# Optimization experiments

Measured on AMD Instinct MI355X. Metric: run time of the kernel, lower is better.

The kernel has to match this reference:

```python
import jax, jax.numpy as jnp
import numpy as np

K, T, D, H = 256, 256, 64, 256
TEMP = 1.0
LOG2 = float(np.log(2.0))


def setup_inputs() -> dict:
    key = jax.random.key(0)
    k1, k2, k3, k4 = jax.random.split(key, 4)
    embeddings_KxtxD = jax.random.normal(k1, (K, T, D), dtype=jnp.float32)
    leaf_counts_Kxt = jax.random.randint(k2, (K, T), 0, 3).astype(jnp.int32)
    W1 = jax.random.normal(k3, (2 * D, H), dtype=jnp.float32) * 0.05
    b1 = jnp.zeros((H,), dtype=jnp.float32)
    W2 = jax.random.normal(k4, (H, D), dtype=jnp.float32) * 0.05
    b2 = jnp.zeros((D,), dtype=jnp.float32)
    return {"N": 256, "leaf_counts_Kxt": leaf_counts_Kxt,
            "embeddings_KxtxD": embeddings_KxtxD, "log": 0,
            "W1": W1, "b1": b1, "W2": W2, "b2": b2}


def _pairwise_dist(emb):  # [K,t,D] -> [K,t,t] Euclidean, no KxtxtxD blowup
    sq = jnp.sum(emb * emb, axis=-1)                       # [K,t]
    gram = jnp.einsum('ktd,ksd->kts', emb, emb)            # [K,t,t]
    d2 = sq[:, :, None] + sq[:, None, :] - 2.0 * gram
    return jnp.sqrt(jnp.maximum(d2, 0.0))


def reference(N, leaf_counts_Kxt, embeddings_KxtxD, log, W1, b1, W2, b2):
    k, t = leaf_counts_Kxt.shape
    dist_Kxtxt = _pairwise_dist(embeddings_KxtxD)
    logw_Kxtxt = -dist_Kxtxt / TEMP
    eye = jnp.eye(t, dtype=bool)
    logw_Kxtxt = jnp.where(eye[None], -jnp.inf, logw_Kxtxt)  # diagonal_scatter(-inf)

    # categorical sample over flattened t*t logits (Gumbel-max)
    skey = jax.random.key(42)
    g = jax.random.gumbel(skey, (k, t * t), dtype=jnp.float32)
    flat_logw = logw_Kxtxt.reshape(k, t * t)
    flat_sample_K = jnp.argmax(flat_logw + g, axis=-1)
    idx1_K = flat_sample_K // t
    idx2_K = flat_sample_K % t

    rows = jnp.arange(k)
    child1_KxD = embeddings_KxtxD[rows, idx1_K]            # gather_K
    child2_KxD = embeddings_KxtxD[rows, idx2_K]

    # merge encoder MLP
    h = jax.nn.relu(jnp.concatenate([child1_KxD, child2_KxD], axis=-1) @ W1 + b1)
    embedding_KxD = h @ W2 + b2

    # sample_branches=False: branch length = distance(child, merged)
    branch1_K = jnp.linalg.norm(child1_KxD - embedding_KxD, axis=-1)
    branch2_K = jnp.linalg.norm(child2_KxD - embedding_KxD, axis=-1)

    log_merge_prob_K = logw_Kxtxt[rows, idx1_K, idx2_K]    # gather_K2
    log_merge_prob_K = log_merge_prob_K + LOG2
    log_merge_prob_K = log_merge_prob_K - jax.scipy.special.logsumexp(
        logw_Kxtxt, axis=(1, 2))
    log_v_plus_K = log_merge_prob_K  # branch priors are 0

    ones_K = jnp.sum((leaf_counts_Kxt == 1).astype(jnp.int32), axis=1)
    ones_K = ones_K - (leaf_counts_Kxt[rows, idx1_K] == 1).astype(jnp.int32)
    ones_K = ones_K - (leaf_counts_Kxt[rows, idx2_K] == 1).astype(jnp.int32)
    v_minus_K = N - ones_K
    log_v_minus_K = jnp.log(v_minus_K.astype(jnp.float32))

    return (idx1_K, idx2_K, branch1_K, branch2_K, embedding_KxD,
            log_v_plus_K, log_v_minus_K)
```

## Files before the change

### kernel.cpp

```cpp
#include <hip/hip_runtime.h>
#include <stdint.h>
#include <math.h>

#define TK 256
#define TT 256
#define DD 64
#define HH 256
#define NTHREADS 1024
#define PADB 72

typedef short bf16x8 __attribute__((ext_vector_type(8)));
typedef float f32x4  __attribute__((ext_vector_type(4)));

struct KWs { unsigned long long packed; float ss; unsigned int arrive; unsigned int pad; };

__device__ __forceinline__ uint32_t rotl32(uint32_t x, uint32_t d) {
  return (x << d) | (x >> (32u - d));
}
__device__ __forceinline__ uint2 threefry2x32(uint32_t x0, uint32_t x1) {
  const uint32_t ks0 = 0u, ks1 = 42u, ks2 = 0x1BD11BF0u;
  x0 += ks0; x1 += ks1;
#define TFR(r) { x0 += x1; x1 = rotl32(x1, r); x1 ^= x0; }
  TFR(13u) TFR(15u) TFR(26u) TFR(6u)
  x0 += ks1; x1 += ks2 + 1u;
  TFR(17u) TFR(29u) TFR(16u) TFR(24u)
  x0 += ks2; x1 += ks0 + 2u;
  TFR(13u) TFR(15u) TFR(26u) TFR(6u)
  x0 += ks0; x1 += ks1 + 3u;
  TFR(17u) TFR(29u) TFR(16u) TFR(24u)
  x0 += ks1; x1 += ks2 + 4u;
  TFR(13u) TFR(15u) TFR(26u) TFR(6u)
  x0 += ks2; x1 += ks0 + 5u;
#undef TFR
  return make_uint2(x0, x1);
}

__device__ __forceinline__ uint16_t f2bf(float x) {
  uint32_t u = __float_as_uint(x);
  return (uint16_t)((u + 0x7FFFu + ((u >> 16) & 1u)) >> 16);
}

__global__ __launch_bounds__(NTHREADS) void ep_fused(
    const int*   __restrict__ pN,
    const int*   __restrict__ leaf,
    const float* __restrict__ emb,
    const float* __restrict__ W1,
    const float* __restrict__ b1,
    const float* __restrict__ W2,
    const float* __restrict__ b2,
    float*       __restrict__ out,
    KWs*         __restrict__ ws)
{
  __shared__ uint16_t s_hi[TT * PADB];
  __shared__ uint16_t s_lo[TT * PADB];
  __shared__ float s_sq[TT];
  __shared__ float s_c1[DD], s_c2[DD];
  __shared__ float s_wss[16], s_wb[16];
  __shared__ int   s_wi[16], s_onesw[16], s_sel[2];
  __shared__ float s_h[HH], s_e[DD];
  __shared__ float s_lse;
  __shared__ int   s_exec;

  const int k    = blockIdx.x >> 1;
  const int half = blockIdx.x & 1;
  const int tid  = threadIdx.x;
  const float* ek = emb + (size_t)k * (TT * DD);

  for (int idx = tid; idx < TT * DD / 4; idx += NTHREADS) {
    float4 v = ((const float4*)ek)[idx];
    int f = idx << 2;
    int r = f >> 6, c = f & 63;
    uint16_t h0 = f2bf(v.x), h1 = f2bf(v.y), h2 = f2bf(v.z), h3 = f2bf(v.w);
    float l0f = v.x - __uint_as_float((uint32_t)h0 << 16);
    float l1f = v.y - __uint_as_float((uint32_t)h1 << 16);
    float l2f = v.z - __uint_as_float((uint32_t)h2 << 16);
    float l3f = v.w - __uint_as_float((uint32_t)h3 << 16);
    uint2 hp = make_uint2((uint32_t)h0 | ((uint32_t)h1 << 16),
                          (uint32_t)h2 | ((uint32_t)h3 << 16));
    uint2 lp = make_uint2((uint32_t)f2bf(l0f) | ((uint32_t)f2bf(l1f) << 16),
                          (uint32_t)f2bf(l2f) | ((uint32_t)f2bf(l3f) << 16));
    *(uint2*)&s_hi[r * PADB + c] = hp;
    *(uint2*)&s_lo[r * PADB + c] = lp;
  }
  if (tid < TT) {
    const float* row = ek + tid * DD;
    float acc = 0.f;
#pragma unroll
    for (int c = 0; c < DD; ++c) acc = fmaf(row[c], row[c], acc);
    s_sq[tid] = acc;
  }
  __syncthreads();

  const int wv = tid >> 6, l = tid & 63;
  const int lm = l & 15, lk = l >> 4;
  const int I0 = wv * 16;

  const char* hib = (const char*)s_hi;
  const char* lob = (const char*)s_lo;
  const int arow = (I0 + lm) * (PADB * 2);
  bf16x8 ah0 = *(const bf16x8*)(hib + arow + lk * 16);
  bf16x8 ah1 = *(const bf16x8*)(hib + arow + 64 + lk * 16);
  bf16x8 al0 = *(const bf16x8*)(lob + arow + lk * 16);
  bf16x8 al1 = *(const bf16x8*)(lob + arow + 64 + lk * 16);

  float sqi_r[4];
#pragma unroll
  for (int r = 0; r < 4; ++r) sqi_r[r] = s_sq[I0 + lk * 4 + r];

  float ss = 0.f, best = -3.402823466e38f;
  int bidx = 0x7fffffff;

  for (int jt = half * 8; jt < half * 8 + 8; ++jt) {
    const int J0 = jt * 16;
    const int brow = (J0 + lm) * (PADB * 2);
    bf16x8 bh0 = *(const bf16x8*)(hib + brow + lk * 16);
    bf16x8 bh1 = *(const bf16x8*)(hib + brow + 64 + lk * 16);
    bf16x8 bl0 = *(const bf16x8*)(lob + brow + lk * 16);
    bf16x8 bl1 = *(const bf16x8*)(lob + brow + 64 + lk * 16);

    f32x4 acc = {0.f, 0.f, 0.f, 0.f};
    acc = __builtin_amdgcn_mfma_f32_16x16x32_bf16(ah0, bh0, acc, 0, 0, 0);
    acc = __builtin_amdgcn_mfma_f32_16x16x32_bf16(ah0, bl0, acc, 0, 0, 0);
    acc = __builtin_amdgcn_mfma_f32_16x16x32_bf16(al0, bh0, acc, 0, 0, 0);
    acc = __builtin_amdgcn_mfma_f32_16x16x32_bf16(ah1, bh1, acc, 0, 0, 0);
    acc = __builtin_amdgcn_mfma_f32_16x16x32_bf16(ah1, bl1, acc, 0, 0, 0);
    acc = __builtin_amdgcn_mfma_f32_16x16x32_bf16(al1, bh1, acc, 0, 0, 0);

    const int j = J0 + lm;
    const float sqj = s_sq[j];
    const uint32_t pbase = ((uint32_t)k << 16) | (uint32_t)j;

#pragma unroll
    for (int r = 0; r < 4; ++r) {
      const int i = I0 + lk * 4 + r;
      float dsq = sqi_r[r] + sqj - 2.0f * acc[r];
      float lw  = -sqrtf(fmaxf(dsq, 0.f));
      if (i != j) {
        ss += __expf(lw);
        uint2 rr = threefry2x32(0u, pbase + ((uint32_t)i << 8));
        uint32_t bits = rr.x ^ rr.y;
        float f = __uint_as_float((bits >> 9) | 0x3F800000u) - 1.0f;
        float u = fmaxf(f, 1.1754943508222875e-38f);
        float g = -__logf(-__logf(u));
        float sv = lw + g;
        int fi = i * TT + j;
        if (sv > best || (sv == best && fi < bidx)) { best = sv; bidx = fi; }
      }
    }
  }

#pragma unroll
  for (int off = 32; off > 0; off >>= 1) {
    ss += __shfl_xor(ss, off);
    float ob = __shfl_xor(best, off);
    int   oi = __shfl_xor(bidx, off);
    if (ob > best || (ob == best && oi < bidx)) { best = ob; bidx = oi; }
  }
  if (l == 0) { s_wss[wv] = ss; s_wb[wv] = best; s_wi[wv] = bidx; }
  {
    int isone = (tid < TT) ? ((leaf[k * TT + tid] == 1) ? 1 : 0) : 0;
    unsigned long long bal = __ballot(isone);
    if (l == 0) s_onesw[wv] = __popcll(bal);
  }
  __syncthreads();

  if (tid == 0) {
    float tot = 0.f, bb = -3.402823466e38f; int bi = 0x7fffffff;
    for (int w = 0; w < 16; ++w) {
      tot += s_wss[w];
      if (s_wb[w] > bb || (s_wb[w] == bb && s_wi[w] < bi)) { bb = s_wb[w]; bi = s_wi[w]; }
    }
    KWs* w = ws + k;
    uint32_t sb = __float_as_uint(bb);
    uint32_t mapped = (sb & 0x80000000u) ? ~sb : (sb | 0x80000000u);
    unsigned long long pk = ((unsigned long long)mapped << 32) |
                            (unsigned long long)(~(uint32_t)bi);
    atomicAdd(&w->ss, tot);
    atomicMax(&w->packed, pk);
    __threadfence();
    unsigned int old = atomicAdd(&w->arrive, 1u);
    if (old == 1u) {
      float tt = atomicAdd(&w->ss, 0.0f);
      unsigned long long fp = atomicMax(&w->packed, 0ull);
      int fbi = (int)(~(uint32_t)(fp & 0xFFFFFFFFull));
      s_sel[0] = fbi >> 8;
      s_sel[1] = fbi & 255;
      s_lse    = logf(tt);
      s_exec   = 1;
    } else {
      s_exec = 0;
    }
  }
  __syncthreads();
  if (!s_exec) return;

  const int i1 = s_sel[0], i2 = s_sel[1];
  if (tid < DD) {
    s_c1[tid] = ek[i1 * DD + tid];
    s_c2[tid] = ek[i2 * DD + tid];
  }
  __syncthreads();

  if (tid < HH) {
    float h0 = 0.f, h1 = 0.f;
#pragma unroll 8
    for (int c = 0; c < DD; ++c) h0 = fmaf(s_c1[c], W1[c * HH + tid], h0);
#pragma unroll 8
    for (int c = 0; c < DD; ++c) h1 = fmaf(s_c2[c], W1[(DD + c) * HH + tid], h1);
    s_h[tid] = fmaxf(h0 + h1 + b1[tid], 0.f);
  }
  __syncthreads();

  if (tid < DD) {
    float acc = 0.f;
#pragma unroll 8
    for (int hh = 0; hh < HH; ++hh) acc = fmaf(s_h[hh], W2[hh * DD + tid], acc);
    float e = acc + b2[tid];
    s_e[tid] = e;
    out[1024 + k * DD + tid] = e;
  }
  __syncthreads();

  if (tid < DD) {
    float dd1 = s_c1[tid] - s_e[tid];
    float dd2 = s_c2[tid] - s_e[tid];
    float q1 = dd1 * dd1, q2 = dd2 * dd2;
#pragma unroll
    for (int off = 32; off > 0; off >>= 1) {
      q1 += __shfl_xor(q1, off);
      q2 += __shfl_xor(q2, off);
    }
    if (tid == 0) {
      out[512 + k] = sqrtf(q1);
      out[768 + k] = sqrtf(q2);
    }
  }

  if (tid == 0) {
    float dot = 0.f;
#pragma unroll
    for (int c = 0; c < DD; ++c) dot = fmaf(s_c1[c], s_c2[c], dot);
    float dsq = s_sq[i1] + s_sq[i2] - 2.0f * dot;
    float lw  = -sqrtf(fmaxf(dsq, 0.f));
    out[0   + k] = (float)i1;
    out[256 + k] = (float)i2;
    out[17408 + k] = lw + 0.69314718055994531f - s_lse;
    int ones = 0;
    for (int w = 0; w < 16; ++w) ones += s_onesw[w];
    ones -= (leaf[k * TT + i1] == 1) ? 1 : 0;
    ones -= (leaf[k * TT + i2] == 1) ? 1 : 0;
    int vminus = pN[0] - ones;
    out[17664 + k] = logf((float)vminus);
  }
}

extern "C" void kernel_launch(void* const* d_in, const int* in_sizes, int n_in,
                              void* d_out, int out_size, void* d_ws, size_t ws_size,
                              hipStream_t stream) {
  const int*   pN   = (const int*)d_in[0];
  const int*   leaf = (const int*)d_in[1];
  const float* emb  = (const float*)d_in[2];
  const float* W1   = (const float*)d_in[4];
  const float* b1   = (const float*)d_in[5];
  const float* W2   = (const float*)d_in[6];
  const float* b2   = (const float*)d_in[7];
  float* out = (float*)d_out;
  KWs*   ws  = (KWs*)d_ws;

  hipMemsetAsync(d_ws, 0, TK * sizeof(KWs), stream);
  ep_fused<<<TK * 2, NTHREADS, 0, stream>>>(pN, leaf, emb, W1, b1, W2, b2, out, ws);
}
```

Before: 150.0 us.

## Batch four MFMA tiles before epilogue and use raw sqrt intrinsic

Restructures the inner loop so that four 16x16 distance tiles are computed by back-to-back MFMA chains into separate accumulators. A scheduling barrier follows, and only then does the threefry/Gumbel epilogue run over all four tiles. The aim is to hide MFMA latency behind independent work and to cut the stalls where each epilogue waited on its own accumulator. It also swaps sqrtf for the raw hardware sqrt intrinsic and adds a min-blocks hint to launch_bounds, both of which can change register allocation. Holding more live accumulators may raise register pressure.

```diff
diff --git a/kernel.cpp b/kernel.cpp
--- a/kernel.cpp
+++ b/kernel.cpp
@@ -40,7 +40,7 @@
   return (uint16_t)((u + 0x7FFFu + ((u >> 16) & 1u)) >> 16);
 }
 
-__global__ __launch_bounds__(NTHREADS) void ep_fused(
+__global__ __launch_bounds__(NTHREADS, 8) void ep_fused(
     const int*   __restrict__ pN,
     const int*   __restrict__ leaf,
     const float* __restrict__ emb,
@@ -110,41 +110,51 @@
   float ss = 0.f, best = -3.402823466e38f;
   int bidx = 0x7fffffff;
 
-  for (int jt = half * 8; jt < half * 8 + 8; ++jt) {
-    const int J0 = jt * 16;
-    const int brow = (J0 + lm) * (PADB * 2);
-    bf16x8 bh0 = *(const bf16x8*)(hib + brow + lk * 16);
-    bf16x8 bh1 = *(const bf16x8*)(hib + brow + 64 + lk * 16);
-    bf16x8 bl0 = *(const bf16x8*)(lob + brow + lk * 16);
-    bf16x8 bl1 = *(const bf16x8*)(lob + brow + 64 + lk * 16);
-
-    f32x4 acc = {0.f, 0.f, 0.f, 0.f};
-    acc = __builtin_amdgcn_mfma_f32_16x16x32_bf16(ah0, bh0, acc, 0, 0, 0);
-    acc = __builtin_amdgcn_mfma_f32_16x16x32_bf16(ah0, bl0, acc, 0, 0, 0);
-    acc = __builtin_amdgcn_mfma_f32_16x16x32_bf16(al0, bh0, acc, 0, 0, 0);
-    acc = __builtin_amdgcn_mfma_f32_16x16x32_bf16(ah1, bh1, acc, 0, 0, 0);
-    acc = __builtin_amdgcn_mfma_f32_16x16x32_bf16(ah1, bl1, acc, 0, 0, 0);
-    acc = __builtin_amdgcn_mfma_f32_16x16x32_bf16(al1, bh1, acc, 0, 0, 0);
-
-    const int j = J0 + lm;
-    const float sqj = s_sq[j];
-    const uint32_t pbase = ((uint32_t)k << 16) | (uint32_t)j;
-
-#pragma unroll
-    for (int r = 0; r < 4; ++r) {
-      const int i = I0 + lk * 4 + r;
-      float dsq = sqi_r[r] + sqj - 2.0f * acc[r];
-      float lw  = -sqrtf(fmaxf(dsq, 0.f));
-      if (i != j) {
-        ss += __expf(lw);
-        uint2 rr = threefry2x32(0u, pbase + ((uint32_t)i << 8));
-        uint32_t bits = rr.x ^ rr.y;
-        float f = __uint_as_float((bits >> 9) | 0x3F800000u) - 1.0f;
-        float u = fmaxf(f, 1.1754943508222875e-38f);
-        float g = -__logf(-__logf(u));
-        float sv = lw + g;
-        int fi = i * TT + j;
-        if (sv > best || (sv == best && fi < bidx)) { best = sv; bidx = fi; }
+  for (int ch = 0; ch < 2; ++ch) {
+    f32x4 acc[4];
+
+#pragma unroll
+    for (int t = 0; t < 4; ++t) {
+      const int J0 = (half * 8 + ch * 4 + t) * 16;
+      const int brow = (J0 + lm) * (PADB * 2);
+      bf16x8 bh0 = *(const bf16x8*)(hib + brow + lk * 16);
+      bf16x8 bh1 = *(const bf16x8*)(hib + brow + 64 + lk * 16);
+      bf16x8 bl0 = *(const bf16x8*)(lob + brow + lk * 16);
+      bf16x8 bl1 = *(const bf16x8*)(lob + brow + 64 + lk * 16);
+      f32x4 a4 = {0.f, 0.f, 0.f, 0.f};
+      a4 = __builtin_amdgcn_mfma_f32_16x16x32_bf16(ah0, bh0, a4, 0, 0, 0);
+      a4 = __builtin_amdgcn_mfma_f32_16x16x32_bf16(ah0, bl0, a4, 0, 0, 0);
+      a4 = __builtin_amdgcn_mfma_f32_16x16x32_bf16(al0, bh0, a4, 0, 0, 0);
+      a4 = __builtin_amdgcn_mfma_f32_16x16x32_bf16(ah1, bh1, a4, 0, 0, 0);
+      a4 = __builtin_amdgcn_mfma_f32_16x16x32_bf16(ah1, bl1, a4, 0, 0, 0);
+      a4 = __builtin_amdgcn_mfma_f32_16x16x32_bf16(al1, bh1, a4, 0, 0, 0);
+      acc[t] = a4;
+    }
+
+    __builtin_amdgcn_sched_barrier(0);
+
+#pragma unroll
+    for (int t = 0; t < 4; ++t) {
+      const int jt = half * 8 + ch * 4 + t;
+      const int j = jt * 16 + lm;
+      const float sqj = s_sq[j];
+      const uint32_t pbase = ((uint32_t)k << 16) | (uint32_t)j;
+#pragma unroll
+      for (int r = 0; r < 4; ++r) {
+        const int i = I0 + lk * 4 + r;
+        float dsq = sqi_r[r] + sqj - 2.0f * acc[t][r];
+        float lw  = -__builtin_amdgcn_sqrtf(fmaxf(dsq, 0.f));
+        if (i != j) {
+          ss += __expf(lw);
+          uint2 rr = threefry2x32(0u, pbase + ((uint32_t)i << 8));
+          uint32_t bits = rr.x ^ rr.y;
+          float f = __uint_as_float((bits >> 9) | 0x3F800000u) - 1.0f;
+          float u = fmaxf(f, 1.1754943508222875e-38f);
+          float g = -__logf(-__logf(u));
+          float sv = lw + g;
+          int fi = i * TT + j;
+          if (sv > best || (sv == best && fi < bidx)) { best = sv; bidx = fi; }
+        }
       }
     }
   }
@@ -267,6 +277,6 @@
   float* out = (float*)d_out;
   KWs*   ws  = (KWs*)d_ws;
 
-  hipMemsetAsync(d_ws, 0, TK * sizeof(KWs), stream);
+  (void)hipMemsetAsync(d_ws, 0, TK * sizeof(KWs), stream);
   ep_fused<<<TK * 2, NTHREADS, 0, stream>>>(pN, leaf, emb, W1, b1, W2, b2, out, ws);
 }
```

New measurement: 146.1 us. 1.03x faster.
